# Kernel optimization log

Measured on AMD Instinct MI355X. Metric: run time of the kernel, lower is better.

The kernel has to match this reference:

```python
import jax, jax.numpy as jnp
import numpy as np

STATE_DIM = 512
HIDDEN = 256
ACTION = 8
BATCH = 32768
LN_EPS = 1e-5


def setup_inputs() -> dict:
    key = jax.random.key(0)
    ks = jax.random.split(key, 24)
    s = 0.02
    inp = {
        'initial_state': jax.random.normal(ks[0], (BATCH, STATE_DIM), jnp.float32),
        'final_state': jax.random.normal(ks[1], (BATCH, STATE_DIM), jnp.float32),
        'horizon': 10,
        # fc: Linear(1024->256), LayerNorm(256), ReLU, Linear(256->256), ReLU
        'W1': jax.random.normal(ks[2], (HIDDEN, 2 * STATE_DIM), jnp.float32) * s,
        'b1': jnp.zeros((HIDDEN,), jnp.float32),
        'ln_g': jnp.ones((HIDDEN,), jnp.float32),
        'ln_b': jnp.zeros((HIDDEN,), jnp.float32),
        'W2': jax.random.normal(ks[3], (HIDDEN, HIDDEN), jnp.float32) * s,
        'b2': jnp.zeros((HIDDEN,), jnp.float32),
        # GRU layer 0 (input=ACTION) and layer 1 (input=HIDDEN)
        'Wih0': jax.random.normal(ks[4], (3 * HIDDEN, ACTION), jnp.float32) * s,
        'Whh0': jax.random.normal(ks[5], (3 * HIDDEN, HIDDEN), jnp.float32) * s,
        'bih0': jnp.zeros((3 * HIDDEN,), jnp.float32),
        'bhh0': jnp.zeros((3 * HIDDEN,), jnp.float32),
        'Wih1': jax.random.normal(ks[6], (3 * HIDDEN, HIDDEN), jnp.float32) * s,
        'Whh1': jax.random.normal(ks[7], (3 * HIDDEN, HIDDEN), jnp.float32) * s,
        'bih1': jnp.zeros((3 * HIDDEN,), jnp.float32),
        'bhh1': jnp.zeros((3 * HIDDEN,), jnp.float32),
        # fc_action: 256 -> 8
        'Wa': jax.random.normal(ks[8], (ACTION, HIDDEN), jnp.float32) * s,
        'ba': jnp.zeros((ACTION,), jnp.float32),
        # fc_init_hidden: 256 -> 512
        'Winit': jax.random.normal(ks[9], (2 * HIDDEN, HIDDEN), jnp.float32) * s,
        'binit': jnp.zeros((2 * HIDDEN,), jnp.float32),
    }
    return inp


def _gru_cell(x, h, Wih, Whh, bih, bhh):
    # torch.nn.GRU cell: gates ordered [r, z, n]
    gi = x @ Wih.T + bih              # [B, 3H]
    gh = h @ Whh.T + bhh              # [B, 3H]
    i_r, i_z, i_n = jnp.split(gi, 3, axis=-1)
    h_r, h_z, h_n = jnp.split(gh, 3, axis=-1)
    r = jax.nn.sigmoid(i_r + h_r)
    z = jax.nn.sigmoid(i_z + h_z)
    n = jnp.tanh(i_n + r * h_n)
    return (1.0 - z) * n + z * h


def reference(initial_state, final_state, horizon, W1, b1, ln_g, ln_b, W2, b2,
              Wih0, Whh0, bih0, bhh0, Wih1, Whh1, bih1, bhh1, Wa, ba, Winit, binit):
    B = initial_state.shape[0]
    combined = jnp.concatenate([initial_state, final_state], axis=-1)  # [B, 2*state]
    h = combined @ W1.T + b1
    mu = jnp.mean(h, axis=-1, keepdims=True)
    var = jnp.var(h, axis=-1, keepdims=True)
    h = (h - mu) * jax.lax.rsqrt(var + LN_EPS) * ln_g + ln_b
    h = jax.nn.relu(h)
    h = jax.nn.relu(h @ W2.T + b2)    # [B, H]

    # Replicates torch .view(2, B, H) on a [B, 2H] tensor (row-major reshape)
    hidden = jnp.reshape(h @ Winit.T + binit, (2, B, HIDDEN))
    h0, h1 = hidden[0], hidden[1]
    a0 = jnp.zeros((B, ACTION), initial_state.dtype)

    def step(carry, _):
        h0, h1, a = carry
        h0n = _gru_cell(a, h0, Wih0, Whh0, bih0, bhh0)
        h1n = _gru_cell(h0n, h1, Wih1, Whh1, bih1, bhh1)
        logits = h1n @ Wa.T + ba       # [B, A]
        a_next = jax.nn.softmax(logits, axis=-1)
        return (h0n, h1n, a_next), logits

    _, logits_seq = jax.lax.scan(step, (h0, h1, a0), None, length=horizon)
    return jnp.transpose(logits_seq, (1, 0, 2))  # [B, horizon, A]
```

## Files before the change

kernel.cpp:

```cpp
#include <hip/hip_runtime.h>


#define HS 264

typedef __attribute__((ext_vector_type(8))) short short8;
typedef __attribute__((ext_vector_type(4))) float fvec4;

__device__ __forceinline__ float bf2f(unsigned short u) {
    union { unsigned int u; float f; } x; x.u = ((unsigned int)u) << 16; return x.f;
}
__device__ __forceinline__ unsigned short f2bf(float f) {
    union { float f; unsigned int u; } x; x.f = f;
    unsigned int r = x.u + 0x7fffu + ((x.u >> 16) & 1u);
    return (unsigned short)(r >> 16);
}
__device__ __forceinline__ float sigm(float x)   { return __builtin_amdgcn_rcpf(1.f + __expf(-x)); }
__device__ __forceinline__ float tanh_f(float x) { return 2.f * __builtin_amdgcn_rcpf(1.f + __expf(-2.f * x)) - 1.f; }

__device__ __forceinline__ short8 ld8(const unsigned short* p) {
    return *reinterpret_cast<const short8*>(p);
}
__device__ __forceinline__ fvec4 mfma16(short8 a, short8 b, fvec4 c) {
    return __builtin_amdgcn_mfma_f32_16x16x32_bf16(a, b, c, 0, 0, 0);
}
__device__ __forceinline__ fvec4 splat4(float v) {
    fvec4 r = {v, v, v, v}; return r;
}

__device__ __forceinline__ int packoff(int e, int K) {
    const int n = e / K, k = e % K;
    return (((n >> 4) * (K >> 5) + (k >> 5)) << 9)
         + (((((k >> 3) & 3) << 4) | (n & 15)) << 3) + (k & 7);
}

__global__ __launch_bounds__(256) void k_prep(
    const float* __restrict__ W1, const float* __restrict__ W2,
    const float* __restrict__ Winit, const float* __restrict__ Wih0,
    const float* __restrict__ Whh0, const float* __restrict__ Wih1,
    const float* __restrict__ Whh1, const float* __restrict__ Wa,
    unsigned short* __restrict__ wb)
{
    int i = blockIdx.x * 256 + threadIdx.x;
    if (i >= 1056768) return;
    float v; int dst;
    if (i < 262144) {
        v = W1[i];                dst = packoff(i, 1024);
    } else if (i < 327680) {
        int e = i - 262144;  v = W2[e];    dst = 262144 + packoff(e, 256);
    } else if (i < 458752) {
        int e = i - 327680;  v = Winit[e]; dst = 327680 + packoff(e, 256);
    } else if (i < 464896) {
        v = Wih0[i - 458752];     dst = i;
    } else if (i < 661504) {
        int e = i - 464896;  v = Whh0[e];  dst = 464896 + packoff(e, 256);
    } else if (i < 858112) {
        int e = i - 661504;  v = Wih1[e];  dst = 661504 + packoff(e, 256);
    } else if (i < 1054720) {
        int e = i - 858112;  v = Whh1[e];  dst = 858112 + packoff(e, 256);
    } else {
        v = Wa[i - 1054720];      dst = i;
    }
    wb[dst] = f2bf(v);
}

__global__ __launch_bounds__(512, 2) void k_encode(
    const float* __restrict__ ini, const float* __restrict__ fin,
    const unsigned short* __restrict__ W1b, const float* __restrict__ b1,
    const float* __restrict__ lng, const float* __restrict__ lnb,
    const unsigned short* __restrict__ W2b, const float* __restrict__ b2,
    const unsigned short* __restrict__ Winitb, const float* __restrict__ binit,
    unsigned short* __restrict__ h0g, unsigned short* __restrict__ h1g)
{
    __shared__ unsigned short hb[64 * HS];
    __shared__ unsigned short at[2][64 * 40];
    __shared__ float ps[64][8][2];
    __shared__ float st[64][2];
    const int tid = threadIdx.x, lane = tid & 63, w = tid >> 6;
    const int l15 = lane & 15, q = lane >> 4;
    const int rows0 = blockIdx.x * 64;
    const int c0 = w * 32;
    const fvec4 fz = {0.f, 0.f, 0.f, 0.f};

    const int srow = tid >> 3, sseg = (tid & 7) * 4;

    fvec4 acc[4][2];
#pragma unroll
    for (int rt = 0; rt < 4; ++rt) { acc[rt][0] = fz; acc[rt][1] = fz; }
    {
        const float* src0 = ini + (rows0 + srow) * 512 + sseg;
        fvec4 v = *reinterpret_cast<const fvec4*>(src0);
        union { unsigned short s[4]; unsigned long long u; } p;
        p.s[0] = f2bf(v[0]); p.s[1] = f2bf(v[1]); p.s[2] = f2bf(v[2]); p.s[3] = f2bf(v[3]);
        *reinterpret_cast<unsigned long long*>(&at[0][srow * 40 + sseg]) = p.u;
    }
    __syncthreads();
#pragma unroll 1
    for (int kc = 0; kc < 32; ++kc) {
        const int buf = kc & 1;
        if (kc < 31) {
            const int k0 = (kc + 1) * 32 + sseg;
            const float* src = (k0 < 512) ? (ini + (rows0 + srow) * 512 + k0)
                                          : (fin + (rows0 + srow) * 512 + (k0 - 512));
            fvec4 v = *reinterpret_cast<const fvec4*>(src);
            union { unsigned short s[4]; unsigned long long u; } p;
            p.s[0] = f2bf(v[0]); p.s[1] = f2bf(v[1]); p.s[2] = f2bf(v[2]); p.s[3] = f2bf(v[3]);
            *reinterpret_cast<unsigned long long*>(&at[buf ^ 1][srow * 40 + sseg]) = p.u;
        }
        short8 b8a = ld8(W1b + (((w * 2 + 0) * 32 + kc) * 64 + lane) * 8);
        short8 b8b = ld8(W1b + (((w * 2 + 1) * 32 + kc) * 64 + lane) * 8);
        short8 a8[4];
#pragma unroll
        for (int rt = 0; rt < 4; ++rt)
            a8[rt] = ld8(&at[buf][(rt * 16 + l15) * 40 + q * 8]);
#pragma unroll
        for (int rt = 0; rt < 4; ++rt) {
            acc[rt][0] = mfma16(a8[rt], b8a, acc[rt][0]);
            acc[rt][1] = mfma16(a8[rt], b8b, acc[rt][1]);
        }
        __syncthreads();
    }
    float bv[2] = { b1[c0 + l15], b1[c0 + 16 + l15] };
#pragma unroll
    for (int rt = 0; rt < 4; ++rt)
#pragma unroll
        for (int r = 0; r < 4; ++r) {
            float s = 0.f, s2 = 0.f;
#pragma unroll
            for (int ct = 0; ct < 2; ++ct) {
                float v = acc[rt][ct][r] + bv[ct];
                acc[rt][ct][r] = v;
                s += v; s2 += v * v;
            }
#pragma unroll
            for (int off = 1; off < 16; off <<= 1) {
                s  += __shfl_xor(s,  off, 64);
                s2 += __shfl_xor(s2, off, 64);
            }
            if (l15 == 0) {
                int row = rt * 16 + q * 4 + r;
                ps[row][w][0] = s; ps[row][w][1] = s2;
            }
        }
    __syncthreads();
    if (tid < 64) {
        float s = 0.f, s2 = 0.f;
#pragma unroll
        for (int j = 0; j < 8; ++j) { s += ps[tid][j][0]; s2 += ps[tid][j][1]; }
        float mu = s * (1.f / 256.f);
        float var = s2 * (1.f / 256.f) - mu * mu;
        st[tid][0] = mu; st[tid][1] = rsqrtf(var + 1e-5f);
    }
    __syncthreads();
    {
        float gv[2]  = { lng[c0 + l15], lng[c0 + 16 + l15] };
        float bbv[2] = { lnb[c0 + l15], lnb[c0 + 16 + l15] };
#pragma unroll
        for (int rt = 0; rt < 4; ++rt)
#pragma unroll
            for (int ct = 0; ct < 2; ++ct)
#pragma unroll
                for (int r = 0; r < 4; ++r) {
                    int row = rt * 16 + q * 4 + r;
                    float v = (acc[rt][ct][r] - st[row][0]) * st[row][1] * gv[ct] + bbv[ct];
                    v = fmaxf(v, 0.f);
                    hb[row * HS + c0 + ct * 16 + l15] = f2bf(v);
                }
    }
    __syncthreads();
    fvec4 acc2[4][2];
#pragma unroll
    for (int rt = 0; rt < 4; ++rt) { acc2[rt][0] = fz; acc2[rt][1] = fz; }
#pragma unroll 2
    for (int kc = 0; kc < 8; ++kc) {
        const int k0 = kc * 32 + q * 8;
        short8 a8[4];
#pragma unroll
        for (int rt = 0; rt < 4; ++rt) a8[rt] = ld8(hb + (rt * 16 + l15) * HS + k0);
#pragma unroll
        for (int ct = 0; ct < 2; ++ct) {
            short8 b8 = ld8(W2b + (((w * 2 + ct) * 8 + kc) * 64 + lane) * 8);
#pragma unroll
            for (int rt = 0; rt < 4; ++rt) acc2[rt][ct] = mfma16(a8[rt], b8, acc2[rt][ct]);
        }
    }
    {
        float b2v[2] = { b2[c0 + l15], b2[c0 + 16 + l15] };
        unsigned short stg[4][2][4];
#pragma unroll
        for (int rt = 0; rt < 4; ++rt)
#pragma unroll
            for (int ct = 0; ct < 2; ++ct)
#pragma unroll
                for (int r = 0; r < 4; ++r)
                    stg[rt][ct][r] = f2bf(fmaxf(acc2[rt][ct][r] + b2v[ct], 0.f));
        __syncthreads();
#pragma unroll
        for (int rt = 0; rt < 4; ++rt)
#pragma unroll
            for (int ct = 0; ct < 2; ++ct)
#pragma unroll
                for (int r = 0; r < 4; ++r)
                    hb[(rt * 16 + q * 4 + r) * HS + c0 + ct * 16 + l15] = stg[rt][ct][r];
    }
    __syncthreads();
    fvec4 a3[4][4];
#pragma unroll
    for (int rt = 0; rt < 4; ++rt)
#pragma unroll
        for (int ct = 0; ct < 4; ++ct) a3[rt][ct] = fz;
#pragma unroll 1
    for (int kc = 0; kc < 8; ++kc) {
        const int k0 = kc * 32 + q * 8;
        short8 a8[4];
#pragma unroll
        for (int rt = 0; rt < 4; ++rt) a8[rt] = ld8(hb + (rt * 16 + l15) * HS + k0);
#pragma unroll
        for (int ct = 0; ct < 4; ++ct) {
            short8 b8 = ld8(Winitb + (((w * 4 + ct) * 8 + kc) * 64 + lane) * 8);
#pragma unroll
            for (int rt = 0; rt < 4; ++rt) a3[rt][ct] = mfma16(a8[rt], b8, a3[rt][ct]);
        }
    }
    const int c0i = w * 64;
#pragma unroll
    for (int ct = 0; ct < 4; ++ct) {
        const int j = c0i + ct * 16 + l15;
        const float bz = binit[j];
        const int half = j >> 8, cc = j & 255;
#pragma unroll
        for (int rt = 0; rt < 4; ++rt)
#pragma unroll
            for (int r = 0; r < 4; ++r) {
                const int i = rows0 + rt * 16 + q * 4 + r;
                const unsigned short v = f2bf(a3[rt][ct][r] + bz);
                if (i < 16384) h0g[(2 * i + half) * 256 + cc] = v;
                else           h1g[(2 * (i - 16384) + half) * 256 + cc] = v;
            }
    }
}

__global__ __launch_bounds__(512, 2) void k_roll(
    const unsigned short* __restrict__ h0g, const unsigned short* __restrict__ h1g,
    const unsigned short* __restrict__ Wih0b, const unsigned short* __restrict__ Whh0b,
    const unsigned short* __restrict__ Wih1b, const unsigned short* __restrict__ Whh1b,
    const unsigned short* __restrict__ Wab,
    const float* __restrict__ bih0, const float* __restrict__ bhh0,
    const float* __restrict__ bih1, const float* __restrict__ bhh1,
    const float* __restrict__ ba, float* __restrict__ out)
{
    __shared__ unsigned short h0sb[2][64 * HS];
    __shared__ unsigned short h1sb[2][64 * HS];
    __shared__ unsigned short avs[64 * 8];
    __shared__ float ldsb[2048];
    const int tid = threadIdx.x, lane = tid & 63, w = tid >> 6;
    const int l15 = lane & 15, q = lane >> 4;
    const int rows0 = blockIdx.x * 64;
    const int cb = w * 32;
    const fvec4 fz = {0.f, 0.f, 0.f, 0.f};
    const short8 z8 = {0,0,0,0,0,0,0,0};

    for (int it = tid; it < 64 * 32; it += 512) {
        const int row = it >> 5, g = (it & 31) * 8;
        *reinterpret_cast<short8*>(&h0sb[0][row * HS + g]) = ld8(h0g + (rows0 + row) * 256 + g);
        *reinterpret_cast<short8*>(&h1sb[0][row * HS + g]) = ld8(h1g + (rows0 + row) * 256 + g);
    }
    if (tid < 256) {
        const int j = tid;
        ldsb[j]       = bih0[j] + bhh0[j];
        ldsb[256 + j] = bih0[256 + j] + bhh0[256 + j];
        ldsb[512 + j] = bih0[512 + j];
        ldsb[768 + j] = bhh0[512 + j];
    } else {
        const int j = tid - 256;
        ldsb[1024 + j] = bih1[j] + bhh1[j];
        ldsb[1280 + j] = bih1[256 + j] + bhh1[256 + j];
        ldsb[1536 + j] = bih1[512 + j];
        ldsb[1792 + j] = bhh1[512 + j];
    }
    const float bav = ba[l15 & 7];
    __syncthreads();

    for (int t = 0; t < 10; ++t) {
        const int cur = t & 1, nxt = cur ^ 1;
        const unsigned short* h0c = h0sb[cur];
        unsigned short*       h0n = h0sb[nxt];
        const unsigned short* h1c = h1sb[cur];
        unsigned short*       h1n = h1sb[nxt];
        {
            fvec4 aR[4][2], aZ[4][2], aNi[4][2], aNh[4][2];
#pragma unroll
            for (int ct = 0; ct < 2; ++ct) {
                const int c = cb + ct * 16 + l15;
                const float vr = ldsb[c],       vz = ldsb[256 + c];
                const float vi = ldsb[512 + c], vh = ldsb[768 + c];
#pragma unroll
                for (int rt = 0; rt < 4; ++rt) {
                    aR[rt][ct]  = splat4(vr);
                    aZ[rt][ct]  = splat4(vz);
                    aNi[rt][ct] = splat4(vi);
                    aNh[rt][ct] = splat4(vh);
                }
            }
#pragma unroll 2
            for (int kc = 0; kc < 8; ++kc) {
                const int k0 = kc * 32 + q * 8;
                short8 wr[2], wz[2], wn[2];
#pragma unroll
                for (int ct = 0; ct < 2; ++ct) {
                    const unsigned short* wp =
                        Whh0b + ((((w * 2 + ct) * 8 + kc) * 64 + lane) * 8);
                    wr[ct] = ld8(wp);
                    wz[ct] = ld8(wp + 65536);
                    wn[ct] = ld8(wp + 131072);
                }
                short8 ah[4];
#pragma unroll
                for (int rt = 0; rt < 4; ++rt)
                    ah[rt] = ld8(h0c + (rt * 16 + l15) * HS + k0);
#pragma unroll
                for (int ct = 0; ct < 2; ++ct)
#pragma unroll
                    for (int rt = 0; rt < 4; ++rt) {
                        aR[rt][ct]  = mfma16(ah[rt], wr[ct], aR[rt][ct]);
                        aZ[rt][ct]  = mfma16(ah[rt], wz[ct], aZ[rt][ct]);
                        aNh[rt][ct] = mfma16(ah[rt], wn[ct], aNh[rt][ct]);
                    }
            }
            if (t > 0) {
                short8 av[4];
#pragma unroll
                for (int rt = 0; rt < 4; ++rt) {
                    short8 v = ld8(avs + (rt * 16 + l15) * 8);
                    av[rt] = (q == 0) ? v : z8;
                }
#pragma unroll
                for (int ct = 0; ct < 2; ++ct) {
                    const unsigned short* wp = Wih0b + (cb + ct * 16 + l15) * 8;
                    short8 wr = ld8(wp);
                    short8 wz = ld8(wp + 2048);
                    short8 wn = ld8(wp + 4096);
#pragma unroll
                    for (int rt = 0; rt < 4; ++rt) {
                        aR[rt][ct]  = mfma16(av[rt], wr, aR[rt][ct]);
                        aZ[rt][ct]  = mfma16(av[rt], wz, aZ[rt][ct]);
                        aNi[rt][ct] = mfma16(av[rt], wn, aNi[rt][ct]);
                    }
                }
            }
#pragma unroll
            for (int ct = 0; ct < 2; ++ct) {
                const int c = cb + ct * 16 + l15;
#pragma unroll
                for (int rt = 0; rt < 4; ++rt)
#pragma unroll
                    for (int r = 0; r < 4; ++r) {
                        const int row = rt * 16 + q * 4 + r;
                        const float hold = bf2f(h0c[row * HS + c]);
                        const float rr = sigm(aR[rt][ct][r]);
                        const float zz = sigm(aZ[rt][ct][r]);
                        const float nn = tanh_f(aNi[rt][ct][r] + rr * aNh[rt][ct][r]);
                        h0n[row * HS + c] = f2bf((1.f - zz) * nn + zz * hold);
                    }
            }
        }
        __syncthreads();
        {
            fvec4 aR[4][2], aZ[4][2], aNi[4][2], aNh[4][2];
#pragma unroll
            for (int ct = 0; ct < 2; ++ct) {
                const int c = cb + ct * 16 + l15;
                const float vr = ldsb[1024 + c], vz = ldsb[1280 + c];
                const float vi = ldsb[1536 + c], vh = ldsb[1792 + c];
#pragma unroll
                for (int rt = 0; rt < 4; ++rt) {
                    aR[rt][ct]  = splat4(vr);
                    aZ[rt][ct]  = splat4(vz);
                    aNi[rt][ct] = splat4(vi);
                    aNh[rt][ct] = splat4(vh);
                }
            }
#pragma unroll 1
            for (int kc = 0; kc < 8; ++kc) {
                const int k0 = kc * 32 + q * 8;
                short8 wir[2], wiz[2], win[2], whr[2], whz[2], whn[2];
#pragma unroll
                for (int ct = 0; ct < 2; ++ct) {
                    const int fo = (((w * 2 + ct) * 8 + kc) * 64 + lane) * 8;
                    const unsigned short* wi = Wih1b + fo;
                    const unsigned short* wh = Whh1b + fo;
                    wir[ct] = ld8(wi);
                    whr[ct] = ld8(wh);
                    wiz[ct] = ld8(wi + 65536);
                    whz[ct] = ld8(wh + 65536);
                    win[ct] = ld8(wi + 131072);
                    whn[ct] = ld8(wh + 131072);
                }
                short8 ai[4], ah[4];
#pragma unroll
                for (int rt = 0; rt < 4; ++rt) {
                    const int rr = (rt * 16 + l15) * HS + k0;
                    ai[rt] = ld8(h0n + rr);
                    ah[rt] = ld8(h1c + rr);
                }
#pragma unroll
                for (int ct = 0; ct < 2; ++ct)
#pragma unroll
                    for (int rt = 0; rt < 4; ++rt) {
                        aR[rt][ct]  = mfma16(ai[rt], wir[ct], aR[rt][ct]);
                        aR[rt][ct]  = mfma16(ah[rt], whr[ct], aR[rt][ct]);
                        aZ[rt][ct]  = mfma16(ai[rt], wiz[ct], aZ[rt][ct]);
                        aZ[rt][ct]  = mfma16(ah[rt], whz[ct], aZ[rt][ct]);
                        aNi[rt][ct] = mfma16(ai[rt], win[ct], aNi[rt][ct]);
                        aNh[rt][ct] = mfma16(ah[rt], whn[ct], aNh[rt][ct]);
                    }
            }
#pragma unroll
            for (int ct = 0; ct < 2; ++ct) {
                const int c = cb + ct * 16 + l15;
#pragma unroll
                for (int rt = 0; rt < 4; ++rt)
#pragma unroll
                    for (int r = 0; r < 4; ++r) {
                        const int row = rt * 16 + q * 4 + r;
                        const float hold = bf2f(h1c[row * HS + c]);
                        const float rr = sigm(aR[rt][ct][r]);
                        const float zz = sigm(aZ[rt][ct][r]);
                        const float nn = tanh_f(aNi[rt][ct][r] + rr * aNh[rt][ct][r]);
                        h1n[row * HS + c] = f2bf((1.f - zz) * nn + zz * hold);
                    }
            }
        }
        __syncthreads();
        if (w < 4) {
            fvec4 f = fz;
#pragma unroll 1
            for (int kc = 0; kc < 8; ++kc) {
                const int k0 = kc * 32 + q * 8;
                short8 a8 = ld8(h1n + (w * 16 + l15) * HS + k0);
                short8 b8 = ld8(Wab + (l15 & 7) * 256 + k0);
                f = mfma16(a8, b8, f);
            }
#pragma unroll
            for (int r = 0; r < 4; ++r) {
                float s = f[r] + bav;
                float m = s;
                m = fmaxf(m, __shfl_xor(m, 1, 64));
                m = fmaxf(m, __shfl_xor(m, 2, 64));
                m = fmaxf(m, __shfl_xor(m, 4, 64));
                float e = __expf(s - m);
                float se = e;
                se += __shfl_xor(se, 1, 64);
                se += __shfl_xor(se, 2, 64);
                se += __shfl_xor(se, 4, 64);
                if (l15 < 8) {
                    const int lrow = w * 16 + q * 4 + r;
                    out[(rows0 + lrow) * 80 + t * 8 + l15] = s;
                    avs[lrow * 8 + l15] = f2bf(e * __builtin_amdgcn_rcpf(se));
                }
            }
        }
        __syncthreads();
    }
}

extern "C" void kernel_launch(void* const* d_in, const int* in_sizes, int n_in,
                              void* d_out, int out_size, void* d_ws, size_t ws_size,
                              hipStream_t stream)
{
    const float* ini   = (const float*)d_in[0];
    const float* fin   = (const float*)d_in[1];
    const float* W1    = (const float*)d_in[3];
    const float* b1    = (const float*)d_in[4];
    const float* lng   = (const float*)d_in[5];
    const float* lnb   = (const float*)d_in[6];
    const float* W2    = (const float*)d_in[7];
    const float* b2    = (const float*)d_in[8];
    const float* Wih0  = (const float*)d_in[9];
    const float* Whh0  = (const float*)d_in[10];
    const float* bih0  = (const float*)d_in[11];
    const float* bhh0  = (const float*)d_in[12];
    const float* Wih1  = (const float*)d_in[13];
    const float* Whh1  = (const float*)d_in[14];
    const float* bih1  = (const float*)d_in[15];
    const float* bhh1  = (const float*)d_in[16];
    const float* Wa    = (const float*)d_in[17];
    const float* ba    = (const float*)d_in[18];
    const float* Winit = (const float*)d_in[19];
    const float* binit = (const float*)d_in[20];
    float* out = (float*)d_out;

    char* ws = (char*)d_ws;
    unsigned short* wb     = (unsigned short*)ws;
    unsigned short* W1b    = wb;
    unsigned short* W2b    = wb + 262144;
    unsigned short* Winitb = wb + 327680;
    unsigned short* Wih0b  = wb + 458752;
    unsigned short* Whh0b  = wb + 464896;
    unsigned short* Wih1b  = wb + 661504;
    unsigned short* Whh1b  = wb + 858112;
    unsigned short* Wab    = wb + 1054720;
    unsigned short* h0g = (unsigned short*)(ws + 2113536);
    unsigned short* h1g = (unsigned short*)(ws + 18890752);

    k_prep<<<dim3(4128), dim3(256), 0, stream>>>(W1, W2, Winit, Wih0, Whh0, Wih1, Whh1, Wa, wb);
    k_encode<<<dim3(512), dim3(512), 0, stream>>>(ini, fin, W1b, b1, lng, lnb, W2b, b2,
                                                  Winitb, binit, h0g, h1g);
    k_roll<<<dim3(512), dim3(512), 0, stream>>>(h0g, h1g, Wih0b, Whh0b, Wih1b, Whh1b, Wab,
                                                bih0, bhh0, bih1, bhh1, ba, out);
}
```

Before: 707.8 us.

## Single-buffer GRU hidden state and shrink per-wave tiles for higher occupancy

```diff
diff --git a/kernel.cpp b/kernel.cpp
--- a/kernel.cpp
+++ b/kernel.cpp
@@ -22,9 +22,6 @@
 }
 __device__ __forceinline__ fvec4 mfma16(short8 a, short8 b, fvec4 c) {
     return __builtin_amdgcn_mfma_f32_16x16x32_bf16(a, b, c, 0, 0, 0);
-}
-__device__ __forceinline__ fvec4 splat4(float v) {
-    fvec4 r = {v, v, v, v}; return r;
 }
 
 __device__ __forceinline__ int packoff(int e, int K) {
@@ -63,7 +60,7 @@
     wb[dst] = f2bf(v);
 }
 
-__global__ __launch_bounds__(512, 2) void k_encode(
+__global__ __launch_bounds__(512, 4) void k_encode(
     const float* __restrict__ ini, const float* __restrict__ fin,
     const unsigned short* __restrict__ W1b, const float* __restrict__ b1,
     const float* __restrict__ lng, const float* __restrict__ lnb,
@@ -239,7 +236,7 @@
     }
 }
 
-__global__ __launch_bounds__(512, 2) void k_roll(
+__global__ __launch_bounds__(512, 4) void k_roll(
     const unsigned short* __restrict__ h0g, const unsigned short* __restrict__ h1g,
     const unsigned short* __restrict__ Wih0b, const unsigned short* __restrict__ Whh0b,
     const unsigned short* __restrict__ Wih1b, const unsigned short* __restrict__ Whh1b,
@@ -248,21 +245,22 @@
     const float* __restrict__ bih1, const float* __restrict__ bhh1,
     const float* __restrict__ ba, float* __restrict__ out)
 {
-    __shared__ unsigned short h0sb[2][64 * HS];
-    __shared__ unsigned short h1sb[2][64 * HS];
+    __shared__ unsigned short h0s[64 * HS];
+    __shared__ unsigned short h1s[64 * HS];
     __shared__ unsigned short avs[64 * 8];
     __shared__ float ldsb[2048];
     const int tid = threadIdx.x, lane = tid & 63, w = tid >> 6;
     const int l15 = lane & 15, q = lane >> 4;
+    const int rowg = (w >> 2) * 32;
+    const int colg = (w & 3) * 16;
     const int rows0 = blockIdx.x * 64;
-    const int cb = w * 32;
     const fvec4 fz = {0.f, 0.f, 0.f, 0.f};
     const short8 z8 = {0,0,0,0,0,0,0,0};
 
     for (int it = tid; it < 64 * 32; it += 512) {
         const int row = it >> 5, g = (it & 31) * 8;
-        *reinterpret_cast<short8*>(&h0sb[0][row * HS + g]) = ld8(h0g + (rows0 + row) * 256 + g);
-        *reinterpret_cast<short8*>(&h1sb[0][row * HS + g]) = ld8(h1g + (rows0 + row) * 256 + g);
+        *reinterpret_cast<short8*>(h0s + row * HS + g) = ld8(h0g + (rows0 + row) * 256 + g);
+        *reinterpret_cast<short8*>(h1s + row * HS + g) = ld8(h1g + (rows0 + row) * 256 + g);
     }
     if (tid < 256) {
         const int j = tid;
@@ -280,163 +278,145 @@
     const float bav = ba[l15 & 7];
     __syncthreads();
 
+#pragma unroll 1
     for (int t = 0; t < 10; ++t) {
-        const int cur = t & 1, nxt = cur ^ 1;
-        const unsigned short* h0c = h0sb[cur];
-        unsigned short*       h0n = h0sb[nxt];
-        const unsigned short* h1c = h1sb[cur];
-        unsigned short*       h1n = h1sb[nxt];
-        {
-            fvec4 aR[4][2], aZ[4][2], aNi[4][2], aNh[4][2];
-#pragma unroll
-            for (int ct = 0; ct < 2; ++ct) {
-                const int c = cb + ct * 16 + l15;
-                const float vr = ldsb[c],       vz = ldsb[256 + c];
-                const float vi = ldsb[512 + c], vh = ldsb[768 + c];
-#pragma unroll
-                for (int rt = 0; rt < 4; ++rt) {
-                    aR[rt][ct]  = splat4(vr);
-                    aZ[rt][ct]  = splat4(vz);
-                    aNi[rt][ct] = splat4(vi);
-                    aNh[rt][ct] = splat4(vh);
-                }
-            }
-#pragma unroll 2
+        unsigned int stash[4][4];
+#pragma unroll 1
+        for (int p = 0; p < 4; ++p) {
+            const int c = p * 64 + colg + l15;
+            const int ntile = p * 4 + (w & 3);
+            fvec4 aR[2], aZ[2], aNi[2], aNh[2];
+#pragma unroll
+            for (int rt = 0; rt < 2; ++rt) { aR[rt]=fz; aZ[rt]=fz; aNi[rt]=fz; aNh[rt]=fz; }
+#pragma unroll 1
+            for (int kc = 0; kc < 8; ++kc) {
+                const unsigned short* wp = Whh0b + ((ntile * 8 + kc) * 64 + lane) * 8;
+                short8 wr = ld8(wp);
+                short8 wz = ld8(wp + 65536);
+                short8 wn = ld8(wp + 131072);
+                const int k0 = kc * 32 + q * 8;
+#pragma unroll
+                for (int rt = 0; rt < 2; ++rt) {
+                    short8 ah = ld8(h0s + (rowg + rt * 16 + l15) * HS + k0);
+                    aR[rt]  = mfma16(ah, wr, aR[rt]);
+                    aZ[rt]  = mfma16(ah, wz, aZ[rt]);
+                    aNh[rt] = mfma16(ah, wn, aNh[rt]);
+                }
+            }
+            if (t > 0) {
+                const unsigned short* wp = Wih0b + c * 8;
+                short8 wr = ld8(wp);
+                short8 wz = ld8(wp + 2048);
+                short8 wn = ld8(wp + 4096);
+#pragma unroll
+                for (int rt = 0; rt < 2; ++rt) {
+                    short8 v = ld8(avs + (rowg + rt * 16 + l15) * 8);
+                    short8 av = (q == 0) ? v : z8;
+                    aR[rt]  = mfma16(av, wr, aR[rt]);
+                    aZ[rt]  = mfma16(av, wz, aZ[rt]);
+                    aNi[rt] = mfma16(av, wn, aNi[rt]);
+                }
+            }
+            const float br = ldsb[c], bz = ldsb[256 + c];
+            const float bi = ldsb[512 + c], bh = ldsb[768 + c];
+#pragma unroll
+            for (int rt = 0; rt < 2; ++rt) {
+                unsigned int p0 = 0, p1 = 0;
+#pragma unroll
+                for (int r = 0; r < 4; ++r) {
+                    const int row = rowg + rt * 16 + q * 4 + r;
+                    const float hold = bf2f(h0s[row * HS + c]);
+                    const float rr = sigm(aR[rt][r] + br);
+                    const float zz = sigm(aZ[rt][r] + bz);
+                    const float nn = tanh_f(aNi[rt][r] + bi + rr * (aNh[rt][r] + bh));
+                    const unsigned int v = f2bf((1.f - zz) * nn + zz * hold);
+                    if (r < 2) p0 |= v << (16 * r); else p1 |= v << (16 * (r - 2));
+                }
+                stash[p][rt * 2]     = p0;
+                stash[p][rt * 2 + 1] = p1;
+            }
+        }
+        __syncthreads();
+#pragma unroll
+        for (int p = 0; p < 4; ++p) {
+            const int c = p * 64 + colg + l15;
+#pragma unroll
+            for (int rt = 0; rt < 2; ++rt)
+#pragma unroll
+                for (int r = 0; r < 4; ++r)
+                    h0s[(rowg + rt * 16 + q * 4 + r) * HS + c] =
+                        (unsigned short)(stash[p][rt * 2 + (r >> 1)] >> (16 * (r & 1)));
+        }
+        __syncthreads();
+#pragma unroll 1
+        for (int p = 0; p < 4; ++p) {
+            const int c = p * 64 + colg + l15;
+            const int ntile = p * 4 + (w & 3);
+            fvec4 aR[2], aZ[2], aNi[2], aNh[2];
+#pragma unroll
+            for (int rt = 0; rt < 2; ++rt) { aR[rt]=fz; aZ[rt]=fz; aNi[rt]=fz; aNh[rt]=fz; }
+#pragma unroll 1
+            for (int kc = 0; kc < 8; ++kc) {
+                const int fo = ((ntile * 8 + kc) * 64 + lane) * 8;
+                const unsigned short* wi = Wih1b + fo;
+                const unsigned short* wh = Whh1b + fo;
+                short8 wir = ld8(wi);
+                short8 whr = ld8(wh);
+                short8 wiz = ld8(wi + 65536);
+                short8 whz = ld8(wh + 65536);
+                short8 win = ld8(wi + 131072);
+                short8 whn = ld8(wh + 131072);
+                const int k0 = kc * 32 + q * 8;
+#pragma unroll
+                for (int rt = 0; rt < 2; ++rt) {
+                    const int rr = (rowg + rt * 16 + l15) * HS + k0;
+                    short8 ai = ld8(h0s + rr);
+                    short8 ah = ld8(h1s + rr);
+                    aR[rt]  = mfma16(ai, wir, aR[rt]);
+                    aR[rt]  = mfma16(ah, whr, aR[rt]);
+                    aZ[rt]  = mfma16(ai, wiz, aZ[rt]);
+                    aZ[rt]  = mfma16(ah, whz, aZ[rt]);
+                    aNi[rt] = mfma16(ai, win, aNi[rt]);
+                    aNh[rt] = mfma16(ah, whn, aNh[rt]);
+                }
+            }
+            const float br = ldsb[1024 + c], bz = ldsb[1280 + c];
+            const float bi = ldsb[1536 + c], bh = ldsb[1792 + c];
+#pragma unroll
+            for (int rt = 0; rt < 2; ++rt) {
+                unsigned int p0 = 0, p1 = 0;
+#pragma unroll
+                for (int r = 0; r < 4; ++r) {
+                    const int row = rowg + rt * 16 + q * 4 + r;
+                    const float hold = bf2f(h1s[row * HS + c]);
+                    const float rr = sigm(aR[rt][r] + br);
+                    const float zz = sigm(aZ[rt][r] + bz);
+                    const float nn = tanh_f(aNi[rt][r] + bi + rr * (aNh[rt][r] + bh));
+                    const unsigned int v = f2bf((1.f - zz) * nn + zz * hold);
+                    if (r < 2) p0 |= v << (16 * r); else p1 |= v << (16 * (r - 2));
+                }
+                stash[p][rt * 2]     = p0;
+                stash[p][rt * 2 + 1] = p1;
+            }
+        }
+        __syncthreads();
+#pragma unroll
+        for (int p = 0; p < 4; ++p) {
+            const int c = p * 64 + colg + l15;
+#pragma unroll
+            for (int rt = 0; rt < 2; ++rt)
+#pragma unroll
+                for (int r = 0; r < 4; ++r)
+                    h1s[(rowg + rt * 16 + q * 4 + r) * HS + c] =
+                        (unsigned short)(stash[p][rt * 2 + (r >> 1)] >> (16 * (r & 1)));
+        }
+        __syncthreads();
+        if (w < 4) {
+            fvec4 f = fz;
+#pragma unroll 1
             for (int kc = 0; kc < 8; ++kc) {
                 const int k0 = kc * 32 + q * 8;
-                short8 wr[2], wz[2], wn[2];
-#pragma unroll
-                for (int ct = 0; ct < 2; ++ct) {
-                    const unsigned short* wp =
-                        Whh0b + ((((w * 2 + ct) * 8 + kc) * 64 + lane) * 8);
-                    wr[ct] = ld8(wp);
-                    wz[ct] = ld8(wp + 65536);
-                    wn[ct] = ld8(wp + 131072);
-                }
-                short8 ah[4];
-#pragma unroll
-                for (int rt = 0; rt < 4; ++rt)
-                    ah[rt] = ld8(h0c + (rt * 16 + l15) * HS + k0);
-#pragma unroll
-                for (int ct = 0; ct < 2; ++ct)
-#pragma unroll
-                    for (int rt = 0; rt < 4; ++rt) {
-                        aR[rt][ct]  = mfma16(ah[rt], wr[ct], aR[rt][ct]);
-                        aZ[rt][ct]  = mfma16(ah[rt], wz[ct], aZ[rt][ct]);
-                        aNh[rt][ct] = mfma16(ah[rt], wn[ct], aNh[rt][ct]);
-                    }
-            }
-            if (t > 0) {
-                short8 av[4];
-#pragma unroll
-                for (int rt = 0; rt < 4; ++rt) {
-                    short8 v = ld8(avs + (rt * 16 + l15) * 8);
-                    av[rt] = (q == 0) ? v : z8;
-                }
-#pragma unroll
-                for (int ct = 0; ct < 2; ++ct) {
-                    const unsigned short* wp = Wih0b + (cb + ct * 16 + l15) * 8;
-                    short8 wr = ld8(wp);
-                    short8 wz = ld8(wp + 2048);
-                    short8 wn = ld8(wp + 4096);
-#pragma unroll
-                    for (int rt = 0; rt < 4; ++rt) {
-                        aR[rt][ct]  = mfma16(av[rt], wr, aR[rt][ct]);
-                        aZ[rt][ct]  = mfma16(av[rt], wz, aZ[rt][ct]);
-                        aNi[rt][ct] = mfma16(av[rt], wn, aNi[rt][ct]);
-                    }
-                }
-            }
-#pragma unroll
-            for (int ct = 0; ct < 2; ++ct) {
-                const int c = cb + ct * 16 + l15;
-#pragma unroll
-                for (int rt = 0; rt < 4; ++rt)
-#pragma unroll
-                    for (int r = 0; r < 4; ++r) {
-                        const int row = rt * 16 + q * 4 + r;
-                        const float hold = bf2f(h0c[row * HS + c]);
-                        const float rr = sigm(aR[rt][ct][r]);
-                        const float zz = sigm(aZ[rt][ct][r]);
-                        const float nn = tanh_f(aNi[rt][ct][r] + rr * aNh[rt][ct][r]);
-                        h0n[row * HS + c] = f2bf((1.f - zz) * nn + zz * hold);
-                    }
-            }
-        }
-        __syncthreads();
-        {
-            fvec4 aR[4][2], aZ[4][2], aNi[4][2], aNh[4][2];
-#pragma unroll
-            for (int ct = 0; ct < 2; ++ct) {
-                const int c = cb + ct * 16 + l15;
-                const float vr = ldsb[1024 + c], vz = ldsb[1280 + c];
-                const float vi = ldsb[1536 + c], vh = ldsb[1792 + c];
-#pragma unroll
-                for (int rt = 0; rt < 4; ++rt) {
-                    aR[rt][ct]  = splat4(vr);
-                    aZ[rt][ct]  = splat4(vz);
-                    aNi[rt][ct] = splat4(vi);
-                    aNh[rt][ct] = splat4(vh);
-                }
-            }
-#pragma unroll 1
-            for (int kc = 0; kc < 8; ++kc) {
-                const int k0 = kc * 32 + q * 8;
-                short8 wir[2], wiz[2], win[2], whr[2], whz[2], whn[2];
-#pragma unroll
-                for (int ct = 0; ct < 2; ++ct) {
-                    const int fo = (((w * 2 + ct) * 8 + kc) * 64 + lane) * 8;
-                    const unsigned short* wi = Wih1b + fo;
-                    const unsigned short* wh = Whh1b + fo;
-                    wir[ct] = ld8(wi);
-                    whr[ct] = ld8(wh);
-                    wiz[ct] = ld8(wi + 65536);
-                    whz[ct] = ld8(wh + 65536);
-                    win[ct] = ld8(wi + 131072);
-                    whn[ct] = ld8(wh + 131072);
-                }
-                short8 ai[4], ah[4];
-#pragma unroll
-                for (int rt = 0; rt < 4; ++rt) {
-                    const int rr = (rt * 16 + l15) * HS + k0;
-                    ai[rt] = ld8(h0n + rr);
-                    ah[rt] = ld8(h1c + rr);
-                }
-#pragma unroll
-                for (int ct = 0; ct < 2; ++ct)
-#pragma unroll
-                    for (int rt = 0; rt < 4; ++rt) {
-                        aR[rt][ct]  = mfma16(ai[rt], wir[ct], aR[rt][ct]);
-                        aR[rt][ct]  = mfma16(ah[rt], whr[ct], aR[rt][ct]);
-                        aZ[rt][ct]  = mfma16(ai[rt], wiz[ct], aZ[rt][ct]);
-                        aZ[rt][ct]  = mfma16(ah[rt], whz[ct], aZ[rt][ct]);
-                        aNi[rt][ct] = mfma16(ai[rt], win[ct], aNi[rt][ct]);
-                        aNh[rt][ct] = mfma16(ah[rt], whn[ct], aNh[rt][ct]);
-                    }
-            }
-#pragma unroll
-            for (int ct = 0; ct < 2; ++ct) {
-                const int c = cb + ct * 16 + l15;
-#pragma unroll
-                for (int rt = 0; rt < 4; ++rt)
-#pragma unroll
-                    for (int r = 0; r < 4; ++r) {
-                        const int row = rt * 16 + q * 4 + r;
-                        const float hold = bf2f(h1c[row * HS + c]);
-                        const float rr = sigm(aR[rt][ct][r]);
-                        const float zz = sigm(aZ[rt][ct][r]);
-                        const float nn = tanh_f(aNi[rt][ct][r] + rr * aNh[rt][ct][r]);
-                        h1n[row * HS + c] = f2bf((1.f - zz) * nn + zz * hold);
-                    }
-            }
-        }
-        __syncthreads();
-        if (w < 4) {
-            fvec4 f = fz;
-#pragma unroll 1
-            for (int kc = 0; kc < 8; ++kc) {
-                const int k0 = kc * 32 + q * 8;
-                short8 a8 = ld8(h1n + (w * 16 + l15) * HS + k0);
+                short8 a8 = ld8(h1s + (w * 16 + l15) * HS + k0);
                 short8 b8 = ld8(Wab + (l15 & 7) * 256 + k0);
                 f = mfma16(a8, b8, f);
             }
```

New measurement: 757.3 us. 7.0% more time.
